# Kernel optimization log

Hardware: AMD Instinct MI355X
Metric: run time of the kernel (lower is better)

Reference implementation:

```python
import jax, jax.numpy as jnp
import numpy as np

T, B, S, V = 50, 64, 400, 50000
D = 512; E = 512; H = 512; A = 512; POOL = 2


def setup_inputs() -> dict:
    key = jax.random.key(0)
    ks = jax.random.split(key, 20)
    def rn(k, shape, s=0.05):
        return jax.random.normal(k, shape, jnp.float32) * s
    return {
        "input_y": jax.random.randint(ks[0], (T, B), 0, V),
        "hidden": rn(ks[1], (1, B, H), 1.0),
        "context": rn(ks[2], (S, B, E), 1.0),
        "src_pad_mask": jnp.zeros((B, S), jnp.float32),
        "init_att": rn(ks[3], (B, E), 1.0),
        "coverage": jnp.zeros((B, S), jnp.float32),
        "global_ctx": rn(ks[4], (B, E), 1.0),
        "emb_W": rn(ks[5], (V, D)).at[0].set(0.0),  # padding_idx=0
        "W_ih": rn(ks[6], (3 * H, D + E)),
        "W_hh": rn(ks[7], (3 * H, H)),
        "b_ih": jnp.zeros((3 * H,), jnp.float32),
        "b_hh": jnp.zeros((3 * H,), jnp.float32),
        "W_pre": rn(ks[8], (E, A)),
        "b_pre": jnp.zeros((A,), jnp.float32),
        "W_q": rn(ks[9], (H + E, A)),
        "W_v": rn(ks[10], (A,)),
        "W_cov": rn(ks[11], (A,)),
        "W_pgen": rn(ks[12], (E + H + D,)),
        "b_pgen": jnp.zeros((), jnp.float32),
        "W_ro": rn(ks[13], (D + H + E + E, H)),
        "b_ro": jnp.zeros((H,), jnp.float32),
    }


def _gru_cell(x, h, W_ih, W_hh, b_ih, b_hh):
    # PyTorch GRUCell gate order: r, z, n
    gi = x @ W_ih.T + b_ih
    gh = h @ W_hh.T + b_hh
    i_r, i_z, i_n = jnp.split(gi, 3, axis=-1)
    h_r, h_z, h_n = jnp.split(gh, 3, axis=-1)
    r = jax.nn.sigmoid(i_r + h_r)
    z = jax.nn.sigmoid(i_z + h_z)
    n = jnp.tanh(i_n + r * h_n)
    return (1.0 - z) * n + z * h


def reference(input_y, hidden, context, src_pad_mask, init_att, coverage, global_ctx,
              emb_W, W_ih, W_hh, b_ih, b_hh, W_pre, b_pre, W_q, W_v, W_cov,
              W_pgen, b_pgen, W_ro, b_ro):
    emb = emb_W[input_y]                      # [T,B,D]
    ctx = jnp.transpose(context, (1, 0, 2))   # [B,S,E]
    precompute = ctx @ W_pre + b_pre          # [B,S,A] (computed once, as in module)
    pad = src_pad_mask > 0.5
    NEG = jnp.float32(-1e18)

    def step(carry, emb_t):
        h, cur_ctx, cov = carry
        x = jnp.concatenate([emb_t, cur_ctx], 1)          # input feed
        h0 = _gru_cell(x, h[0], W_ih, W_hh, b_ih, b_hh)   # layers=1
        h = h.at[0].set(h0)
        output = h0
        # concat attention with coverage
        q = jnp.concatenate([output, global_ctx], 1) @ W_q          # [B,A]
        tmp = jnp.tanh(precompute + q[:, None, :] + cov[..., None] * W_cov)
        energy = tmp @ W_v                                           # [B,S]
        energy = jnp.where(pad, NEG, energy)
        attn = jax.nn.softmax(energy, axis=1)
        cur_ctx = jnp.einsum('bs,bse->be', attn, ctx)
        # pointer-gen
        p_gen = jax.nn.sigmoid(
            jnp.concatenate([cur_ctx, output, emb_t], 1) @ W_pgen + b_pgen)[:, None]
        # readout + maxout (dropout is identity in eval)
        readout = jnp.concatenate([emb_t, output, cur_ctx, global_ctx], 1) @ W_ro + b_ro
        mo = readout.reshape(B, H // POOL, POOL).max(axis=-1)        # [B,H/POOL]
        cov_loss = jnp.sum(jnp.minimum(attn, cov), 1)                # cov_loss_wt=1.0
        next_cov = cov + attn
        return (h, cur_ctx, next_cov), (mo, p_gen, attn, cov_loss)

    (hidden_f, cur_ctx_f, cov_f), (g_out, g_pg, g_attn, cov_losses) = jax.lax.scan(
        step, (hidden, init_att, coverage), emb)
    return (g_out, hidden_f, g_attn[-1], cur_ctx_f, g_pg, g_attn, cov_losses, cov_f)
```

## Files before the change

### kernel.cpp

```cpp
#include <hip/hip_runtime.h>
#include <hip/hip_bf16.h>


#define T_STEPS 50
#define BB 64
#define SS 400

#define O_GOUT 0
#define O_HID 819200
#define O_ATTN_LAST 851968
#define O_CTXF 877568
#define O_PG 910336
#define O_GATTN 913536
#define O_COVL 2193536
#define O_COVF 2196736

typedef __attribute__((ext_vector_type(4))) float f4;
typedef __attribute__((ext_vector_type(8))) short s8v;
typedef __attribute__((ext_vector_type(4))) unsigned u4;

static __device__ __forceinline__ float bf2f(unsigned short u){
  unsigned v = ((unsigned)u) << 16; return __builtin_bit_cast(float, v);
}
static __device__ __forceinline__ unsigned short f2bf(float f){
  unsigned u = __builtin_bit_cast(unsigned, f);
  unsigned r = (u + 0x7FFFu + ((u >> 16) & 1u)) >> 16;
  return (unsigned short)r;
}
static __device__ __forceinline__ float sigmoidf_(float x){ return 1.f/(1.f+__expf(-x)); }
static __device__ __forceinline__ float tanhf_(float x){ float e=__expf(2.f*x); return 1.f - 2.f/(e+1.f); }
static __device__ __forceinline__ u4 ntld(const unsigned short* p){
  return __builtin_nontemporal_load((const u4*)p);
}

__global__ void conv_ctx(const float* __restrict__ ctx, unsigned short* __restrict__ out){
  int o = blockIdx.x*256 + threadIdx.x;
  if(o >= SS*BB*512) return;
  int e = o & 511; int b = (o>>9)&63; int s = o>>15;
  out[((b*SS+s)<<9) + e] = f2bf(ctx[o]);
}
__global__ void conv_emb(const int* __restrict__ y, const float* __restrict__ embW,
                         unsigned short* __restrict__ embU){
  int o = blockIdx.x*256+threadIdx.x; if(o>=T_STEPS*BB*512) return;
  int d = o & 511; int i = o>>9;
  embU[o] = f2bf(embW[(long)y[i]*512 + d]);
}
__global__ void conv_rest(const float* __restrict__ W_ih, const float* __restrict__ W_hh,
                          const float* __restrict__ W_pre, const float* __restrict__ W_ro,
                          const float* __restrict__ W_q,
                          const float* __restrict__ hidden, const float* __restrict__ init_att,
                          const float* __restrict__ gctx, const float* __restrict__ coverage,
                          unsigned short* __restrict__ wihbf, unsigned short* __restrict__ wpreT,
                          unsigned short* __restrict__ wroT, unsigned short* __restrict__ Wgru,
                          unsigned short* __restrict__ WqP,
                          float* __restrict__ hrow0, unsigned short* __restrict__ h0bf_init,
                          unsigned short* __restrict__ ctx0bf, float* __restrict__ gctxT,
                          float* __restrict__ cov){
  int o = blockIdx.x*256+threadIdx.x;
  if(o < 786432){
    int j = o>>9; int d = o&511;
    wihbf[o] = f2bf(W_ih[(long)j*1024 + d]);
  } else if(o < 1048576){
    int p = o - 786432;
    int a = p>>9; int e = p&511;
    wpreT[p] = f2bf(W_pre[(long)e*512 + a]);
  } else if(o < 2097152){
    int p = o - 1048576;
    int n = p>>11; int k = p&2047;
    wroT[p] = f2bf(W_ro[(long)k*512 + n]);
  } else if(o < 3670016){
    int p = o - 2097152;
    int rg = p >> 13; int rem = p & 8191;
    int ki = rem >> 9; int ln = (rem >> 3) & 63; int e = p & 7;
    int blk = rg/24; int r2 = rg%24; int w = r2/6; int r3 = r2%6; int g = r3>>1; int op = r3&1;
    int rl = ln & 15; int kk = ((ln>>4)<<3) + e;
    int d = blk*64 + w*16 + rl; int j = g*512 + d; int k = ki*32 + kk;
    float v = op ? W_hh[(long)j*512 + k] : W_ih[(long)j*1024 + 512 + k];
    Wgru[p] = f2bf(v);
  } else if(o < 3932160){
    int p = o - 3670016;
    int e = p&7; int ln=(p>>3)&63; int kf=(p>>9)&1; int nrg=(p>>10)&31; int blk=p>>15;
    int n = nrg*16 + (ln&15);
    int k = blk*64 + kf*32 + ((ln>>4)<<3) + e;
    WqP[p] = f2bf(W_q[(long)k*512 + n]);
  } else if(o < 4056064){
    int p = o - 3932160;
    if(p < 32768){ float v = hidden[p]; hrow0[p] = v; h0bf_init[p] = f2bf(v); }
    else if(p < 65536){ int q=p-32768; ctx0bf[q] = f2bf(init_att[q]); }
    else if(p < 98304){ int q=p-65536; int b=q>>9,e=q&511; gctxT[e*64+b]=gctx[q]; }
    else { int q=p-98304; cov[q]=coverage[q]; }
  }
}

template<int OUT_BF16>
__global__ __launch_bounds__(256) void mfma_gemm(
    const unsigned short* __restrict__ Abf, int lda,
    const unsigned short* __restrict__ Bbf, int ldb,
    void* __restrict__ Cp, int ldc, const float* __restrict__ bias, int K)
{
  __shared__ __align__(16) unsigned short Ash[128*40];
  __shared__ __align__(16) unsigned short Bsh[128*40];
  int m0 = blockIdx.x*128, n0 = blockIdx.y*128;
  int tid = threadIdx.x;
  int wid = tid>>6, lane = tid&63;
  int wm = wid>>1, wn = wid&1;
  int lr = lane&15, lg = lane>>4;
  f4 acc[4][4];
  #pragma unroll
  for(int i=0;i<4;i++)
    #pragma unroll
    for(int j=0;j<4;j++) acc[i][j]=(f4)0.f;

  for(int kt=0; kt<K; kt+=32){
    #pragma unroll
    for(int c=0;c<2;c++){
      int flat = tid*16 + c*8;
      int row = flat>>5, col = flat&31;
      const unsigned short* ga = Abf + (long)(m0+row)*lda + kt + col;
      *(uint4*)(&Ash[row*40+col]) = *(const uint4*)ga;
      const unsigned short* gb = Bbf + (long)(n0+row)*ldb + kt + col;
      *(uint4*)(&Bsh[row*40+col]) = *(const uint4*)gb;
    }
    __syncthreads();
    s8v av[4], bv[4];
    #pragma unroll
    for(int mi=0;mi<4;mi++) av[mi] = *(const s8v*)(&Ash[(wm*64+mi*16+lr)*40 + lg*8]);
    #pragma unroll
    for(int ni=0;ni<4;ni++) bv[ni] = *(const s8v*)(&Bsh[(wn*64+ni*16+lr)*40 + lg*8]);
    #pragma unroll
    for(int mi=0;mi<4;mi++)
      #pragma unroll
      for(int ni=0;ni<4;ni++)
        acc[mi][ni] = __builtin_amdgcn_mfma_f32_16x16x32_bf16(av[mi], bv[ni], acc[mi][ni], 0,0,0);
    __syncthreads();
  }
  #pragma unroll
  for(int mi=0;mi<4;mi++)
    #pragma unroll
    for(int ni=0;ni<4;ni++){
      int gc = n0 + wn*64 + ni*16 + lr;
      #pragma unroll
      for(int r=0;r<4;r++){
        int gr = m0 + wm*64 + mi*16 + lg*4 + r;
        float v = acc[mi][ni][r];
        if(bias) v += bias[gc];
        if(OUT_BF16) ((unsigned short*)Cp)[(long)gr*ldc + gc] = f2bf(v);
        else         ((float*)Cp)[(long)gr*ldc + gc] = v;
      }
    }
}

__global__ __launch_bounds__(256) void mfma_gemm_ro(
    const unsigned short* __restrict__ embU, const unsigned short* __restrict__ h0bf,
    const unsigned short* __restrict__ ctxA, const unsigned short* __restrict__ wroT,
    float* __restrict__ RO, const float* __restrict__ bias)
{
  __shared__ __align__(16) unsigned short Ash[128*40];
  __shared__ __align__(16) unsigned short Bsh[128*40];
  int m0 = blockIdx.x*128, n0 = blockIdx.y*128;
  int tid = threadIdx.x;
  int wid = tid>>6, lane = tid&63;
  int wm = wid>>1, wn = wid&1;
  int lr = lane&15, lg = lane>>4;
  f4 acc[4][4];
  #pragma unroll
  for(int i=0;i<4;i++)
    #pragma unroll
    for(int j=0;j<4;j++) acc[i][j]=(f4)0.f;

  for(int kt=0; kt<1536; kt+=32){
    const unsigned short* src = (kt<512) ? embU : (kt<1024) ? h0bf : ctxA;
    int klocal = kt & 511;
    #pragma unroll
    for(int c=0;c<2;c++){
      int flat = tid*16 + c*8;
      int row = flat>>5, col = flat&31;
      *(uint4*)(&Ash[row*40+col]) = *(const uint4*)(src + (long)(m0+row)*512 + klocal + col);
      *(uint4*)(&Bsh[row*40+col]) = *(const uint4*)(wroT + (long)(n0+row)*2048 + kt + col);
    }
    __syncthreads();
    s8v av[4], bv[4];
    #pragma unroll
    for(int mi=0;mi<4;mi++) av[mi] = *(const s8v*)(&Ash[(wm*64+mi*16+lr)*40 + lg*8]);
    #pragma unroll
    for(int ni=0;ni<4;ni++) bv[ni] = *(const s8v*)(&Bsh[(wn*64+ni*16+lr)*40 + lg*8]);
    #pragma unroll
    for(int mi=0;mi<4;mi++)
      #pragma unroll
      for(int ni=0;ni<4;ni++)
        acc[mi][ni] = __builtin_amdgcn_mfma_f32_16x16x32_bf16(av[mi], bv[ni], acc[mi][ni], 0,0,0);
    __syncthreads();
  }
  #pragma unroll
  for(int mi=0;mi<4;mi++)
    #pragma unroll
    for(int ni=0;ni<4;ni++){
      int gc = n0 + wn*64 + ni*16 + lr;
      #pragma unroll
      for(int r=0;r<4;r++){
        int gr = m0 + wm*64 + mi*16 + lg*4 + r;
        RO[(long)gr*512 + gc] = acc[mi][ni][r] + bias[gc];
      }
    }
}

__global__ __launch_bounds__(256) void small2(
  const float* __restrict__ AT, const float* __restrict__ W_q, const float* __restrict__ W_ro,
  float* __restrict__ q_g, float* __restrict__ ro_g)
{
  int blk = blockIdx.x;
  int half = blk>>7; int nblk = blk&127;
  int tid = threadIdx.x;
  int b = tid&63; int nq = tid>>6;
  int n = __builtin_amdgcn_readfirstlane(nblk*4 + nq);
  const float* W = half ? W_ro : W_q;
  int koff = half ? 1536 : 512;
  float acc = 0.f;
  const float* wp = W + (long)koff*512 + n;
  #pragma unroll 8
  for(int k=0;k<512;k++){
    acc = fmaf(AT[k*64+b], wp[(long)k*512], acc);
  }
  (half ? ro_g : q_g)[b*512+n] = acc;
}

__global__ __launch_bounds__(256) void k_gru3(
  const unsigned short* __restrict__ ctx0bf, const float* __restrict__ ctxP,
  const float* __restrict__ S_part, const float* __restrict__ P_exp,
  const unsigned short* __restrict__ hprevbf,
  const float* __restrict__ hrow_in, float* __restrict__ hrow_out,
  const unsigned short* __restrict__ Wp, const unsigned short* __restrict__ WqP,
  const float* __restrict__ gi_emb, const float* __restrict__ b_hh,
  unsigned short* __restrict__ h0bf_all, float* __restrict__ qpart,
  float* __restrict__ cov, unsigned short* __restrict__ ctxA,
  float* __restrict__ outp, int t)
{
  __shared__ __align__(16) unsigned short Ash[2*64*256];
  __shared__ __align__(16) unsigned short HS[64*72];
  __shared__ float invS[64];
  __shared__ float red[256];
  int blk = blockIdx.x;
  int tid = threadIdx.x;
  int w = tid>>6, lane = tid&63;
  int lr = lane&15, lg = lane>>4;

  if(blk >= 8){
    if(t==0) return;
    int b = blk-8; int tb = t-1;
    float S = S_part[b*4]+S_part[b*4+1]+S_part[b*4+2]+S_part[b*4+3];
    float inv = 1.f/S;
    float clp;
    {
      float p = P_exp[b*400+tid];
      float attn = p*inv;
      float co = cov[b*400+tid];
      clp = fminf(attn, co);
      cov[b*400+tid] = co+attn;
      outp[O_GATTN + (long)tb*25600 + b*400 + tid] = attn;
    }
    if(tid<144){
      int i = 256+tid;
      float p = P_exp[b*400+i];
      float attn = p*inv;
      float co = cov[b*400+i];
      clp += fminf(attn, co);
      cov[b*400+i] = co+attn;
      outp[O_GATTN + (long)tb*25600 + b*400 + i] = attn;
    }
    red[tid]=clp; __syncthreads();
    for(int o=128;o;o>>=1){ if(tid<o) red[tid]+=red[tid+o]; __syncthreads(); }
    if(tid==0) outp[O_COVL + tb*64 + b] = red[0];
    return;
  }

  int swz = (lr&7)<<4;
  int rgbase = blk*24 + w*6;
  if(t>0 && tid<64){
    float S = S_part[tid*4]+S_part[tid*4+1]+S_part[tid*4+2]+S_part[tid*4+3];
    invS[tid] = 1.f/S;
  }
  __syncthreads();

  f4 acc2[6][4];
  #pragma unroll
  for(int u=0;u<6;u++)
    #pragma unroll
    for(int mi=0;mi<4;mi++) acc2[u][mi]=(f4)0.f;

  for(int kp=0; kp<2; kp++){
    for(int c = tid; c < 4096; c += 256){
      int op = c>>11; int row = (c>>5)&63; int kc = c&31;
      int e0 = kp*256 + kc*8;
      u4 v;
      if(op){
        v = *(const u4*)(hprevbf + row*512 + e0);
      } else if(t>0){
        const float* cp = ctxP + (long)row*2048 + e0;
        float sc = invS[row];
        f4 a0 = *(const f4*)(cp);
        f4 a1 = *(const f4*)(cp+512);
        f4 a2 = *(const f4*)(cp+1024);
        f4 a3 = *(const f4*)(cp+1536);
        f4 b0 = *(const f4*)(cp+4);
        f4 b1 = *(const f4*)(cp+516);
        f4 b2 = *(const f4*)(cp+1028);
        f4 b3 = *(const f4*)(cp+1540);
        f4 s0 = (a0+a1+a2+a3)*sc;
        f4 s1 = (b0+b1+b2+b3)*sc;
        v.x = (unsigned)f2bf(s0.x) | ((unsigned)f2bf(s0.y)<<16);
        v.y = (unsigned)f2bf(s0.z) | ((unsigned)f2bf(s0.w)<<16);
        v.z = (unsigned)f2bf(s1.x) | ((unsigned)f2bf(s1.y)<<16);
        v.w = (unsigned)f2bf(s1.z) | ((unsigned)f2bf(s1.w)<<16);
        if(blk == (row>>3))
          *(u4*)(ctxA + ((long)((t-1)*64+row))*512 + e0) = v;
      } else {
        v = *(const u4*)(ctx0bf + row*512 + e0);
      }
      int dst = op*32768 + row*512 + ((kc*16) ^ ((row&7)<<4));
      *(u4*)((char*)Ash + dst) = v;
    }
    __syncthreads();
    #pragma unroll 2
    for(int ktl=0; ktl<256; ktl+=32){
      s8v av[2][4];
      #pragma unroll
      for(int op=0;op<2;op++)
        #pragma unroll
        for(int mi=0;mi<4;mi++)
          av[op][mi] = *(const s8v*)((const char*)Ash + op*32768 + (mi*16+lr)*512 + ((ktl*2 + lg*16) ^ swz));
      int ki = kp*8 + (ktl>>5);
      const unsigned short* wb = Wp + (long)rgbase*8192 + ki*512 + lane*8;
      #pragma unroll
      for(int u=0;u<6;u++){
        s8v bv = *(const s8v*)(wb + (long)u*8192);
        #pragma unroll
        for(int mi=0;mi<4;mi++)
          acc2[u][mi] = __builtin_amdgcn_mfma_f32_16x16x32_bf16(av[u&1][mi], bv, acc2[u][mi], 0,0,0);
      }
    }
    __syncthreads();
  }

  int d = blk*64 + w*16 + lr;
  float bhr = b_hh[d], bhz = b_hh[512+d], bhn = b_hh[1024+d];
  #pragma unroll
  for(int mi=0;mi<4;mi++){
    #pragma unroll
    for(int r=0;r<4;r++){
      int b = mi*16 + lg*4 + r;
      const float* ge = gi_emb + (long)(t*64+b)*1536;
      float g0 = __builtin_nontemporal_load(ge + d);
      float g1 = __builtin_nontemporal_load(ge + 512 + d);
      float g2 = __builtin_nontemporal_load(ge + 1024 + d);
      float rr = sigmoidf_(g0 + bhr + acc2[0][mi][r] + acc2[1][mi][r]);
      float zz = sigmoidf_(g1 + bhz + acc2[2][mi][r] + acc2[3][mi][r]);
      float nn = tanhf_(  g2       + acc2[4][mi][r] + rr*(acc2[5][mi][r] + bhn));
      float hp = hrow_in[b*512 + d];
      float hv = (1.f-zz)*nn + zz*hp;
      hrow_out[b*512+d] = hv;
      unsigned short hb = f2bf(hv);
      h0bf_all[(long)(t*64+b)*512 + d] = hb;
      HS[b*72 + w*16 + lr] = hb;
      if(t==T_STEPS-1) outp[O_HID + b*512 + d] = hv;
    }
  }
  __syncthreads();
  #pragma unroll
  for(int i=0;i<8;i++){
    f4 accq[4];
    #pragma unroll
    for(int mi=0;mi<4;mi++) accq[mi]=(f4)0.f;
    #pragma unroll
    for(int kf=0;kf<2;kf++){
      s8v bv = *(const s8v*)(WqP + ((((long)blk*32 + (w*8+i))*2 + kf)*64 + lane)*8);
      #pragma unroll
      for(int mi=0;mi<4;mi++){
        s8v av = *(const s8v*)(HS + (mi*16+lr)*72 + kf*32 + lg*8);
        accq[mi] = __builtin_amdgcn_mfma_f32_16x16x32_bf16(av, bv, accq[mi], 0,0,0);
      }
    }
    int n = w*128 + i*16 + lr;
    #pragma unroll
    for(int mi=0;mi<4;mi++)
      #pragma unroll
      for(int r=0;r<4;r++)
        qpart[(long)blk*32768 + (long)(mi*16+lg*4+r)*512 + n] = accq[mi][r];
  }
}

__global__ __launch_bounds__(512) void k_energy2(
  const unsigned short* __restrict__ pre, const float* __restrict__ qpart,
  const float* __restrict__ q_g, const float* __restrict__ cov,
  const float* __restrict__ Wv, const float* __restrict__ Wcov,
  const float* __restrict__ padm, const unsigned short* __restrict__ ctxbf,
  float* __restrict__ P_exp, float* __restrict__ S_part, float* __restrict__ ctxP)
{
  __shared__ float q_sh[512], wv_sh[512], wc_sh[512];
  __shared__ float covL[104], padL[104], pL[104];
  __shared__ float pb[8][512];
  __shared__ float red2[8];
  int cq = blockIdx.x, b = blockIdx.y; int c0 = cq*100;
  int tid = threadIdx.x, w = tid>>6, lane = tid&63;
  {
    float acc = q_g[b*512+tid];
    #pragma unroll
    for(int p=0;p<8;p++) acc += qpart[((long)p<<15) + b*512 + tid];
    q_sh[tid] = acc;
    wv_sh[tid] = Wv[tid]; wc_sh[tid] = Wcov[tid];
    if(tid<100){ covL[tid]=cov[b*400+c0+tid]; padL[tid]=padm[b*400+c0+tid]; }
  }
  __syncthreads();
  float wsum = 0.f;
  int i = w;
  u4 pf = {0,0,0,0};
  if(i<100) pf = ntld(pre + (((long)(b*400+c0+i))<<9) + lane*8);
  while(i<100){
    u4 cur = pf;
    int nx = i+8;
    if(nx<100) pf = ntld(pre + (((long)(b*400+c0+nx))<<9) + lane*8);
    float cv = covL[i];
    float part = 0.f;
    int a0 = lane*8;
    #pragma unroll
    for(int q4=0;q4<4;q4++){
      unsigned uu = (q4==0)?cur.x:(q4==1)?cur.y:(q4==2)?cur.z:cur.w;
      int a = a0 + q4*2;
      part += wv_sh[a]  * tanhf_(bf2f((unsigned short)(uu&0xffffu)) + q_sh[a]   + cv*wc_sh[a]);
      part += wv_sh[a+1]* tanhf_(bf2f((unsigned short)(uu>>16))    + q_sh[a+1] + cv*wc_sh[a+1]);
    }
    #pragma unroll
    for(int off=32;off;off>>=1) part += __shfl_xor(part, off, 64);
    if(lane==0){
      float e = (padL[i]>0.5f) ? -1e18f : part;
      float p = __expf(e);
      pL[i] = p;
      P_exp[b*400+c0+i] = p;
      wsum += p;
    }
    i = nx;
  }
  if(lane==0) red2[w]=wsum;
  __syncthreads();
  if(tid==0)
    S_part[b*4+cq] = red2[0]+red2[1]+red2[2]+red2[3]+red2[4]+red2[5]+red2[6]+red2[7];
  float acc8[8];
  #pragma unroll
  for(int j=0;j<8;j++) acc8[j]=0.f;
  i = w;
  u4 cf = {0,0,0,0};
  if(i<100) cf = ntld(ctxbf + (((long)(b*400+c0+i))<<9) + lane*8);
  while(i<100){
    u4 cur = cf;
    int nx = i+8;
    if(nx<100) cf = ntld(ctxbf + (((long)(b*400+c0+nx))<<9) + lane*8);
    float pv = pL[i];
    acc8[0] = fmaf(pv, bf2f((unsigned short)(cur.x&0xffffu)), acc8[0]);
    acc8[1] = fmaf(pv, bf2f((unsigned short)(cur.x>>16)),     acc8[1]);
    acc8[2] = fmaf(pv, bf2f((unsigned short)(cur.y&0xffffu)), acc8[2]);
    acc8[3] = fmaf(pv, bf2f((unsigned short)(cur.y>>16)),     acc8[3]);
    acc8[4] = fmaf(pv, bf2f((unsigned short)(cur.z&0xffffu)), acc8[4]);
    acc8[5] = fmaf(pv, bf2f((unsigned short)(cur.z>>16)),     acc8[5]);
    acc8[6] = fmaf(pv, bf2f((unsigned short)(cur.w&0xffffu)), acc8[6]);
    acc8[7] = fmaf(pv, bf2f((unsigned short)(cur.w>>16)),     acc8[7]);
    i = nx;
  }
  f4 v0 = {acc8[0],acc8[1],acc8[2],acc8[3]};
  f4 v1 = {acc8[4],acc8[5],acc8[6],acc8[7]};
  *(f4*)(&pb[w][lane*8])   = v0;
  *(f4*)(&pb[w][lane*8+4]) = v1;
  __syncthreads();
  {
    float v = pb[0][tid]+pb[1][tid]+pb[2][tid]+pb[3][tid]
             +pb[4][tid]+pb[5][tid]+pb[6][tid]+pb[7][tid];
    ctxP[((long)b*4+cq)*512 + tid] = v;
  }
}

__global__ __launch_bounds__(256) void k_fin(
  const float* __restrict__ ctxP, const float* __restrict__ S_part,
  const float* __restrict__ P_exp, const float* __restrict__ cov,
  unsigned short* __restrict__ ctxA, float* __restrict__ outp)
{
  __shared__ float red[256];
  int b = blockIdx.x; int tid = threadIdx.x;
  const int tb = T_STEPS-1;
  float S = S_part[b*4]+S_part[b*4+1]+S_part[b*4+2]+S_part[b*4+3];
  float inv = 1.f/S;
  float clp;
  {
    float p = P_exp[b*400+tid]; float attn = p*inv;
    float co = cov[b*400+tid];
    clp = fminf(attn, co);
    float nc = co+attn;
    outp[O_GATTN + (long)tb*25600 + b*400 + tid] = attn;
    outp[O_ATTN_LAST + b*400 + tid] = attn;
    outp[O_COVF + b*400 + tid] = nc;
  }
  if(tid<144){
    int i = 256+tid;
    float p = P_exp[b*400+i]; float attn = p*inv;
    float co = cov[b*400+i];
    clp += fminf(attn, co);
    float nc = co+attn;
    outp[O_GATTN + (long)tb*25600 + b*400 + i] = attn;
    outp[O_ATTN_LAST + b*400 + i] = attn;
    outp[O_COVF + b*400 + i] = nc;
  }
  red[tid]=clp; __syncthreads();
  for(int o=128;o;o>>=1){ if(tid<o) red[tid]+=red[tid+o]; __syncthreads(); }
  if(tid==0) outp[O_COVL + tb*64 + b] = red[0];
  for(int c=tid;c<512;c+=256){
    float v = (ctxP[(long)b*2048+c]+ctxP[(long)b*2048+512+c]
              +ctxP[(long)b*2048+1024+c]+ctxP[(long)b*2048+1536+c])*inv;
    outp[O_CTXF + b*512 + c] = v;
    ctxA[(long)(tb*64+b)*512 + c] = f2bf(v);
  }
}

__global__ __launch_bounds__(256) void k_post(
  const unsigned short* __restrict__ embU, const unsigned short* __restrict__ h0bf,
  const unsigned short* __restrict__ ctxA, const float* __restrict__ Wpg,
  const float* __restrict__ bpg, const float* __restrict__ RO,
  const float* __restrict__ ro_g, float* __restrict__ outp)
{
  int blk = blockIdx.x;
  if(blk < 800){
    int wid = threadIdx.x>>6, lane=threadIdx.x&63;
    int m = blk*4 + wid;
    float acc=0.f;
    #pragma unroll
    for(int i=0;i<8;i++){
      int k = i*64+lane;
      acc = fmaf(bf2f(ctxA[(long)m*512+k]), Wpg[k], acc);
      acc = fmaf(bf2f(h0bf[(long)m*512+k]), Wpg[512+k], acc);
      acc = fmaf(bf2f(embU[(long)m*512+k]), Wpg[1024+k], acc);
    }
    #pragma unroll
    for(int off=32; off; off>>=1) acc += __shfl_xor(acc, off, 64);
    if(lane==0) outp[O_PG + m] = sigmoidf_(acc + bpg[0]);
  } else {
    int o = (blk-800)*256 + threadIdx.x;
    int h = o & 255; int m = o>>8; int b = m & 63;
    float v0 = RO[(long)m*512 + 2*h]   + ro_g[b*512 + 2*h];
    float v1 = RO[(long)m*512 + 2*h+1] + ro_g[b*512 + 2*h+1];
    outp[O_GOUT + o] = fmaxf(v0,v1);
  }
}

extern "C" void kernel_launch(void* const* d_in, const int* in_sizes, int n_in,
                              void* d_out, int out_size, void* d_ws, size_t ws_size,
                              hipStream_t stream)
{
  (void)in_sizes; (void)n_in; (void)out_size; (void)ws_size;
  const int*   y       = (const int*)d_in[0];
  const float* hidden  = (const float*)d_in[1];
  const float* context = (const float*)d_in[2];
  const float* padm    = (const float*)d_in[3];
  const float* init_att= (const float*)d_in[4];
  const float* coverage= (const float*)d_in[5];
  const float* gctx    = (const float*)d_in[6];
  const float* embW    = (const float*)d_in[7];
  const float* W_ih    = (const float*)d_in[8];
  const float* W_hh    = (const float*)d_in[9];
  const float* b_ih    = (const float*)d_in[10];
  const float* b_hh    = (const float*)d_in[11];
  const float* W_pre   = (const float*)d_in[12];
  const float* b_pre   = (const float*)d_in[13];
  const float* W_q     = (const float*)d_in[14];
  const float* W_v     = (const float*)d_in[15];
  const float* W_cov   = (const float*)d_in[16];
  const float* W_pg    = (const float*)d_in[17];
  const float* b_pg    = (const float*)d_in[18];
  const float* W_ro    = (const float*)d_in[19];
  const float* b_ro    = (const float*)d_in[20];
  float* out = (float*)d_out;

  char* wsb = (char*)d_ws;
  size_t off = 0;
  auto alloc = [&](size_t bytes)->char*{ char* p = wsb+off; off += (bytes+255)&~255UL; return p; };
  unsigned short* pre    = (unsigned short*)alloc(25600UL*512*2);
  unsigned short* ctxbf  = (unsigned short*)alloc(13107200UL*2);
  unsigned short* embU   = (unsigned short*)alloc(3200UL*512*2);
  unsigned short* wihbf  = (unsigned short*)alloc(1536UL*512*2);
  unsigned short* wpreT  = (unsigned short*)alloc(512UL*512*2);
  unsigned short* wroT   = (unsigned short*)alloc(512UL*2048*2);
  unsigned short* Wgru   = (unsigned short*)alloc(192UL*8192*2);
  unsigned short* WqP    = (unsigned short*)alloc(262144UL*2);
  float* gi_emb = (float*)alloc(3200UL*1536*4);
  float* RO     = (float*)alloc(3200UL*512*4);
  float* q_g    = (float*)alloc(64UL*512*4);
  float* ro_g   = (float*)alloc(64UL*512*4);
  float* hrow0  = (float*)alloc(64UL*512*4);
  float* hrow1  = (float*)alloc(64UL*512*4);
  float* gctxT  = (float*)alloc(512UL*64*4);
  unsigned short* h0bf = (unsigned short*)alloc(3200UL*512*2);
  unsigned short* h0bf_init = (unsigned short*)alloc(64UL*512*2);
  unsigned short* ctx0bf    = (unsigned short*)alloc(64UL*512*2);
  unsigned short* ctxA = (unsigned short*)alloc(3200UL*512*2);
  float* ctxP   = (float*)alloc(64UL*4*512*4);
  float* P_exp  = (float*)alloc(64UL*400*4);
  float* S_part = (float*)alloc(64UL*4*4);
  float* qpart  = (float*)alloc(8UL*64*512*4);
  float* cov    = (float*)alloc(64UL*400*4);

  conv_ctx <<<dim3(51200),dim3(256),0,stream>>>(context, ctxbf);
  conv_emb <<<dim3(6400), dim3(256),0,stream>>>(y, embW, embU);
  conv_rest<<<dim3(15844),dim3(256),0,stream>>>(W_ih, W_hh, W_pre, W_ro, W_q,
                                                hidden, init_att, gctx, coverage,
                                                wihbf, wpreT, wroT, Wgru, WqP,
                                                hrow0, h0bf_init, ctx0bf, gctxT, cov);

  mfma_gemm<1><<<dim3(200,4),dim3(256),0,stream>>>(ctxbf,512, wpreT,512,  pre,   512, b_pre, 512);
  mfma_gemm<0><<<dim3(25,12),dim3(256),0,stream>>>(embU, 512, wihbf,512,  gi_emb,1536, b_ih, 512);
  small2<<<dim3(256),dim3(256),0,stream>>>(gctxT, W_q, W_ro, q_g, ro_g);

  for(int t=0; t<T_STEPS; t++){
    float* hin  = (t&1) ? hrow1 : hrow0;
    float* hout = (t&1) ? hrow0 : hrow1;
    const unsigned short* hprevbf = t ? (h0bf + (long)(t-1)*32768) : h0bf_init;
    k_gru3<<<dim3(72),dim3(256),0,stream>>>(ctx0bf, ctxP, S_part, P_exp, hprevbf,
                                            hin, hout, Wgru, WqP, gi_emb, b_hh,
                                            h0bf, qpart, cov, ctxA, out, t);
    k_energy2<<<dim3(4,64),dim3(512),0,stream>>>(pre, qpart, q_g, cov, W_v, W_cov,
                                                 padm, ctxbf, P_exp, S_part, ctxP);
  }

  k_fin<<<dim3(64),dim3(256),0,stream>>>(ctxP, S_part, P_exp, cov, ctxA, out);
  mfma_gemm_ro<<<dim3(25,4),dim3(256),0,stream>>>(embU, h0bf, ctxA, wroT, RO, b_ro);
  k_post<<<dim3(4000),dim3(256),0,stream>>>(embU, h0bf, ctxA, W_pg, b_pg, RO, ro_g, out);
}
```

Measured before the change: 3.011 ms.

## Fuse GRU and attention-energy kernels into one per-step launch with flag sync

Merges the per-step GRU kernel and the attention energy kernel into a single 264-block launch. The 8 GRU blocks publish the query partials and signal completion through an atomic per-step flag, while the 256 attention blocks spin-wait on that flag. The coverage update and coverage-loss work moves into the attention blocks, and S_part is double-buffered so readers of the previous step do not race the current writers. This halves the kernel launches inside the step loop and overlaps the coverage work with the GRU. In exchange it relies on all blocks being co-resident, and a spin-wait with a timeout break could deadlock or silently continue if they are not.

```diff
diff --git a/kernel.cpp b/kernel.cpp
--- a/kernel.cpp
+++ b/kernel.cpp
@@ -29,8 +29,13 @@
 }
 static __device__ __forceinline__ float sigmoidf_(float x){ return 1.f/(1.f+__expf(-x)); }
 static __device__ __forceinline__ float tanhf_(float x){ float e=__expf(2.f*x); return 1.f - 2.f/(e+1.f); }
-static __device__ __forceinline__ u4 ntld(const unsigned short* p){
-  return __builtin_nontemporal_load((const u4*)p);
+static __device__ __forceinline__ float ald32f(const float* p){
+  unsigned u = __hip_atomic_load((const unsigned*)p, __ATOMIC_RELAXED, __HIP_MEMORY_SCOPE_AGENT);
+  return __builtin_bit_cast(float, u);
+}
+static __device__ __forceinline__ void ast32f(float* p, float v){
+  __hip_atomic_store((unsigned*)p, __builtin_bit_cast(unsigned, v),
+                     __ATOMIC_RELAXED, __HIP_MEMORY_SCOPE_AGENT);
 }
 
 __global__ void conv_ctx(const float* __restrict__ ctx, unsigned short* __restrict__ out){
@@ -55,7 +60,7 @@
                           unsigned short* __restrict__ WqP,
                           float* __restrict__ hrow0, unsigned short* __restrict__ h0bf_init,
                           unsigned short* __restrict__ ctx0bf, float* __restrict__ gctxT,
-                          float* __restrict__ cov){
+                          float* __restrict__ cov, unsigned* __restrict__ flags){
   int o = blockIdx.x*256+threadIdx.x;
   if(o < 786432){
     int j = o>>9; int d = o&511;
@@ -83,12 +88,13 @@
     int n = nrg*16 + (ln&15);
     int k = blk*64 + kf*32 + ((ln>>4)<<3) + e;
     WqP[p] = f2bf(W_q[(long)k*512 + n]);
-  } else if(o < 4056064){
+  } else if(o < 4056128){
     int p = o - 3932160;
     if(p < 32768){ float v = hidden[p]; hrow0[p] = v; h0bf_init[p] = f2bf(v); }
     else if(p < 65536){ int q=p-32768; ctx0bf[q] = f2bf(init_att[q]); }
     else if(p < 98304){ int q=p-65536; int b=q>>9,e=q&511; gctxT[e*64+b]=gctx[q]; }
-    else { int q=p-98304; cov[q]=coverage[q]; }
+    else if(p < 123904){ int q=p-98304; cov[q]=coverage[q]; }
+    else { int q=p-123904; if(q<64) flags[q]=0u; }
   }
 }
 
@@ -224,291 +230,299 @@
   (half ? ro_g : q_g)[b*512+n] = acc;
 }
 
-__global__ __launch_bounds__(256) void k_gru3(
-  const unsigned short* __restrict__ ctx0bf, const float* __restrict__ ctxP,
-  const float* __restrict__ S_part, const float* __restrict__ P_exp,
+__global__ __launch_bounds__(512) void k_step(
+  const unsigned short* __restrict__ ctx0bf, float* __restrict__ ctxP,
+  float* __restrict__ S_part, float* __restrict__ P_exp,
   const unsigned short* __restrict__ hprevbf,
   const float* __restrict__ hrow_in, float* __restrict__ hrow_out,
   const unsigned short* __restrict__ Wp, const unsigned short* __restrict__ WqP,
   const float* __restrict__ gi_emb, const float* __restrict__ b_hh,
   unsigned short* __restrict__ h0bf_all, float* __restrict__ qpart,
   float* __restrict__ cov, unsigned short* __restrict__ ctxA,
+  const unsigned short* __restrict__ pre, const unsigned short* __restrict__ ctxbf,
+  const float* __restrict__ q_g, const float* __restrict__ Wv,
+  const float* __restrict__ Wcov, const float* __restrict__ padm,
+  float* __restrict__ covl_part, unsigned* __restrict__ flags,
   float* __restrict__ outp, int t)
 {
-  __shared__ __align__(16) unsigned short Ash[2*64*256];
-  __shared__ __align__(16) unsigned short HS[64*72];
-  __shared__ float invS[64];
-  __shared__ float red[256];
-  int blk = blockIdx.x;
-  int tid = threadIdx.x;
-  int w = tid>>6, lane = tid&63;
-  int lr = lane&15, lg = lane>>4;
-
-  if(blk >= 8){
-    if(t==0) return;
-    int b = blk-8; int tb = t-1;
-    float S = S_part[b*4]+S_part[b*4+1]+S_part[b*4+2]+S_part[b*4+3];
-    float inv = 1.f/S;
-    float clp;
-    {
-      float p = P_exp[b*400+tid];
-      float attn = p*inv;
-      float co = cov[b*400+tid];
-      clp = fminf(attn, co);
-      cov[b*400+tid] = co+attn;
-      outp[O_GATTN + (long)tb*25600 + b*400 + tid] = attn;
-    }
-    if(tid<144){
-      int i = 256+tid;
-      float p = P_exp[b*400+i];
-      float attn = p*inv;
-      float co = cov[b*400+i];
-      clp += fminf(attn, co);
-      cov[b*400+i] = co+attn;
-      outp[O_GATTN + (long)tb*25600 + b*400 + i] = attn;
-    }
-    red[tid]=clp; __syncthreads();
-    for(int o=128;o;o>>=1){ if(tid<o) red[tid]+=red[tid+o]; __syncthreads(); }
-    if(tid==0) outp[O_COVL + tb*64 + b] = red[0];
-    return;
-  }
-
-  int swz = (lr&7)<<4;
-  int rgbase = blk*24 + w*6;
-  if(t>0 && tid<64){
-    float S = S_part[tid*4]+S_part[tid*4+1]+S_part[tid*4+2]+S_part[tid*4+3];
-    invS[tid] = 1.f/S;
-  }
-  __syncthreads();
-
-  f4 acc2[6][4];
-  #pragma unroll
-  for(int u=0;u<6;u++)
-    #pragma unroll
-    for(int mi=0;mi<4;mi++) acc2[u][mi]=(f4)0.f;
-
-  for(int kp=0; kp<2; kp++){
-    for(int c = tid; c < 4096; c += 256){
-      int op = c>>11; int row = (c>>5)&63; int kc = c&31;
-      int e0 = kp*256 + kc*8;
-      u4 v;
-      if(op){
-        v = *(const u4*)(hprevbf + row*512 + e0);
-      } else if(t>0){
-        const float* cp = ctxP + (long)row*2048 + e0;
-        float sc = invS[row];
-        f4 a0 = *(const f4*)(cp);
-        f4 a1 = *(const f4*)(cp+512);
-        f4 a2 = *(const f4*)(cp+1024);
-        f4 a3 = *(const f4*)(cp+1536);
-        f4 b0 = *(const f4*)(cp+4);
-        f4 b1 = *(const f4*)(cp+516);
-        f4 b2 = *(const f4*)(cp+1028);
-        f4 b3 = *(const f4*)(cp+1540);
-        f4 s0 = (a0+a1+a2+a3)*sc;
-        f4 s1 = (b0+b1+b2+b3)*sc;
-        v.x = (unsigned)f2bf(s0.x) | ((unsigned)f2bf(s0.y)<<16);
-        v.y = (unsigned)f2bf(s0.z) | ((unsigned)f2bf(s0.w)<<16);
-        v.z = (unsigned)f2bf(s1.x) | ((unsigned)f2bf(s1.y)<<16);
-        v.w = (unsigned)f2bf(s1.z) | ((unsigned)f2bf(s1.w)<<16);
-        if(blk == (row>>3))
-          *(u4*)(ctxA + ((long)((t-1)*64+row))*512 + e0) = v;
-      } else {
-        v = *(const u4*)(ctx0bf + row*512 + e0);
-      }
-      int dst = op*32768 + row*512 + ((kc*16) ^ ((row&7)<<4));
-      *(u4*)((char*)Ash + dst) = v;
-    }
-    __syncthreads();
-    #pragma unroll 2
-    for(int ktl=0; ktl<256; ktl+=32){
-      s8v av[2][4];
-      #pragma unroll
-      for(int op=0;op<2;op++)
+  __shared__ __align__(16) char smem[75008];
+  const int blk = blockIdx.x;
+  const int tid = threadIdx.x;
+  const int w = tid>>6, lane = tid&63;
+  const int lr = lane&15, lg = lane>>4;
+
+  if(blk < 8){
+    unsigned short* Ash = (unsigned short*)smem;
+    unsigned short* HS  = (unsigned short*)(smem+65536);
+    float* invS = (float*)(smem+74752);
+    const int swz = (lr&7)<<4;
+    const int rgbase = blk*24 + w*6;
+
+    if(t>0 && tid<64){
+      const float* Sp = S_part + ((t-1)&1)*256 + tid*4;
+      invS[tid] = 1.f/(Sp[0]+Sp[1]+Sp[2]+Sp[3]);
+    }
+    __syncthreads();
+
+    f4 acc2[6][4];
+    #pragma unroll
+    for(int u=0;u<6;u++)
+      #pragma unroll
+      for(int mi=0;mi<4;mi++) acc2[u][mi]=(f4)0.f;
+
+    for(int kp=0; kp<2; kp++){
+      for(int c = tid; c < 4096; c += 512){
+        int op = c>>11; int row = (c>>5)&63; int kc = c&31;
+        int e0 = kp*256 + kc*8;
+        u4 v;
+        if(op){
+          v = *(const u4*)(hprevbf + row*512 + e0);
+        } else if(t>0){
+          const float* cp = ctxP + (long)row*2048 + e0;
+          float sc = invS[row];
+          f4 a0 = *(const f4*)(cp);
+          f4 a1 = *(const f4*)(cp+512);
+          f4 a2 = *(const f4*)(cp+1024);
+          f4 a3 = *(const f4*)(cp+1536);
+          f4 b0 = *(const f4*)(cp+4);
+          f4 b1 = *(const f4*)(cp+516);
+          f4 b2 = *(const f4*)(cp+1028);
+          f4 b3 = *(const f4*)(cp+1540);
+          f4 s0 = (a0+a1+a2+a3)*sc;
+          f4 s1 = (b0+b1+b2+b3)*sc;
+          v.x = (unsigned)f2bf(s0.x) | ((unsigned)f2bf(s0.y)<<16);
+          v.y = (unsigned)f2bf(s0.z) | ((unsigned)f2bf(s0.w)<<16);
+          v.z = (unsigned)f2bf(s1.x) | ((unsigned)f2bf(s1.y)<<16);
+          v.w = (unsigned)f2bf(s1.z) | ((unsigned)f2bf(s1.w)<<16);
+          if(blk == (row>>3))
+            *(u4*)(ctxA + ((long)((t-1)*64+row))*512 + e0) = v;
+        } else {
+          v = *(const u4*)(ctx0bf + row*512 + e0);
+        }
+        int dst = op*32768 + row*512 + ((kc*16) ^ ((row&7)<<4));
+        *(u4*)((char*)Ash + dst) = v;
+      }
+      __syncthreads();
+      if(w<4){
+        #pragma unroll 2
+        for(int ktl=0; ktl<256; ktl+=32){
+          s8v av[2][4];
+          #pragma unroll
+          for(int op=0;op<2;op++)
+            #pragma unroll
+            for(int mi=0;mi<4;mi++)
+              av[op][mi] = *(const s8v*)((const char*)Ash + op*32768 + (mi*16+lr)*512 + ((ktl*2 + lg*16) ^ swz));
+          int ki = kp*8 + (ktl>>5);
+          const unsigned short* wb = Wp + (long)rgbase*8192 + ki*512 + lane*8;
+          #pragma unroll
+          for(int u=0;u<6;u++){
+            s8v bv = *(const s8v*)(wb + (long)u*8192);
+            #pragma unroll
+            for(int mi=0;mi<4;mi++)
+              acc2[u][mi] = __builtin_amdgcn_mfma_f32_16x16x32_bf16(av[u&1][mi], bv, acc2[u][mi], 0,0,0);
+          }
+        }
+      }
+      __syncthreads();
+    }
+
+    if(w<4){
+      int d = blk*64 + w*16 + lr;
+      float bhr = b_hh[d], bhz = b_hh[512+d], bhn = b_hh[1024+d];
+      #pragma unroll
+      for(int mi=0;mi<4;mi++){
+        #pragma unroll
+        for(int r=0;r<4;r++){
+          int b = mi*16 + lg*4 + r;
+          const float* ge = gi_emb + (long)(t*64+b)*1536;
+          float g0 = __builtin_nontemporal_load(ge + d);
+          float g1 = __builtin_nontemporal_load(ge + 512 + d);
+          float g2 = __builtin_nontemporal_load(ge + 1024 + d);
+          float rr = sigmoidf_(g0 + bhr + acc2[0][mi][r] + acc2[1][mi][r]);
+          float zz = sigmoidf_(g1 + bhz + acc2[2][mi][r] + acc2[3][mi][r]);
+          float nn = tanhf_(  g2       + acc2[4][mi][r] + rr*(acc2[5][mi][r] + bhn));
+          float hp = hrow_in[b*512 + d];
+          float hv = (1.f-zz)*nn + zz*hp;
+          hrow_out[b*512+d] = hv;
+          unsigned short hb = f2bf(hv);
+          h0bf_all[(long)(t*64+b)*512 + d] = hb;
+          HS[b*72 + w*16 + lr] = hb;
+          if(t==T_STEPS-1) outp[O_HID + b*512 + d] = hv;
+        }
+      }
+    }
+    __syncthreads();
+    if(w<4){
+      #pragma unroll
+      for(int i=0;i<8;i++){
+        f4 accq[4];
+        #pragma unroll
+        for(int mi=0;mi<4;mi++) accq[mi]=(f4)0.f;
+        #pragma unroll
+        for(int kf=0;kf<2;kf++){
+          s8v bv = *(const s8v*)(WqP + ((((long)blk*32 + (w*8+i))*2 + kf)*64 + lane)*8);
+          #pragma unroll
+          for(int mi=0;mi<4;mi++){
+            s8v av = *(const s8v*)(HS + (mi*16+lr)*72 + kf*32 + lg*8);
+            accq[mi] = __builtin_amdgcn_mfma_f32_16x16x32_bf16(av, bv, accq[mi], 0,0,0);
+          }
+        }
+        int n = w*128 + i*16 + lr;
         #pragma unroll
         for(int mi=0;mi<4;mi++)
-          av[op][mi] = *(const s8v*)((const char*)Ash + op*32768 + (mi*16+lr)*512 + ((ktl*2 + lg*16) ^ swz));
-      int ki = kp*8 + (ktl>>5);
-      const unsigned short* wb = Wp + (long)rgbase*8192 + ki*512 + lane*8;
-      #pragma unroll
-      for(int u=0;u<6;u++){
-        s8v bv = *(const s8v*)(wb + (long)u*8192);
-        #pragma unroll
-        for(int mi=0;mi<4;mi++)
-          acc2[u][mi] = __builtin_amdgcn_mfma_f32_16x16x32_bf16(av[u&1][mi], bv, acc2[u][mi], 0,0,0);
-      }
-    }
-    __syncthreads();
-  }
-
-  int d = blk*64 + w*16 + lr;
-  float bhr = b_hh[d], bhz = b_hh[512+d], bhn = b_hh[1024+d];
-  #pragma unroll
-  for(int mi=0;mi<4;mi++){
-    #pragma unroll
-    for(int r=0;r<4;r++){
-      int b = mi*16 + lg*4 + r;
-      const float* ge = gi_emb + (long)(t*64+b)*1536;
-      float g0 = __builtin_nontemporal_load(ge + d);
-      float g1 = __builtin_nontemporal_load(ge + 512 + d);
-      float g2 = __builtin_nontemporal_load(ge + 1024 + d);
-      float rr = sigmoidf_(g0 + bhr + acc2[0][mi][r] + acc2[1][mi][r]);
-      float zz = sigmoidf_(g1 + bhz + acc2[2][mi][r] + acc2[3][mi][r]);
-      float nn = tanhf_(  g2       + acc2[4][mi][r] + rr*(acc2[5][mi][r] + bhn));
-      float hp = hrow_in[b*512 + d];
-      float hv = (1.f-zz)*nn + zz*hp;
-      hrow_out[b*512+d] = hv;
-      unsigned short hb = f2bf(hv);
-      h0bf_all[(long)(t*64+b)*512 + d] = hb;
-      HS[b*72 + w*16 + lr] = hb;
-      if(t==T_STEPS-1) outp[O_HID + b*512 + d] = hv;
-    }
-  }
-  __syncthreads();
-  #pragma unroll
-  for(int i=0;i<8;i++){
-    f4 accq[4];
-    #pragma unroll
-    for(int mi=0;mi<4;mi++) accq[mi]=(f4)0.f;
-    #pragma unroll
-    for(int kf=0;kf<2;kf++){
-      s8v bv = *(const s8v*)(WqP + ((((long)blk*32 + (w*8+i))*2 + kf)*64 + lane)*8);
-      #pragma unroll
-      for(int mi=0;mi<4;mi++){
-        s8v av = *(const s8v*)(HS + (mi*16+lr)*72 + kf*32 + lg*8);
-        accq[mi] = __builtin_amdgcn_mfma_f32_16x16x32_bf16(av, bv, accq[mi], 0,0,0);
-      }
-    }
-    int n = w*128 + i*16 + lr;
-    #pragma unroll
-    for(int mi=0;mi<4;mi++)
-      #pragma unroll
-      for(int r=0;r<4;r++)
-        qpart[(long)blk*32768 + (long)(mi*16+lg*4+r)*512 + n] = accq[mi][r];
-  }
-}
-
-__global__ __launch_bounds__(512) void k_energy2(
-  const unsigned short* __restrict__ pre, const float* __restrict__ qpart,
-  const float* __restrict__ q_g, const float* __restrict__ cov,
-  const float* __restrict__ Wv, const float* __restrict__ Wcov,
-  const float* __restrict__ padm, const unsigned short* __restrict__ ctxbf,
-  float* __restrict__ P_exp, float* __restrict__ S_part, float* __restrict__ ctxP)
-{
-  __shared__ float q_sh[512], wv_sh[512], wc_sh[512];
-  __shared__ float covL[104], padL[104], pL[104];
-  __shared__ float pb[8][512];
-  __shared__ float red2[8];
-  int cq = blockIdx.x, b = blockIdx.y; int c0 = cq*100;
-  int tid = threadIdx.x, w = tid>>6, lane = tid&63;
+          #pragma unroll
+          for(int r=0;r<4;r++)
+            ast32f(qpart + (long)blk*32768 + (long)(mi*16+lg*4+r)*512 + n, accq[mi][r]);
+      }
+    }
+    asm volatile("s_waitcnt vmcnt(0)" ::: "memory");
+    __syncthreads();
+    if(tid==0)
+      __hip_atomic_fetch_add(flags+t, 1u, __ATOMIC_RELEASE, __HIP_MEMORY_SCOPE_AGENT);
+    return;
+  }
+
   {
-    float acc = q_g[b*512+tid];
-    #pragma unroll
-    for(int p=0;p<8;p++) acc += qpart[((long)p<<15) + b*512 + tid];
-    q_sh[tid] = acc;
-    wv_sh[tid] = Wv[tid]; wc_sh[tid] = Wcov[tid];
-    if(tid<100){ covL[tid]=cov[b*400+c0+tid]; padL[tid]=padm[b*400+c0+tid]; }
-  }
-  __syncthreads();
-  float wsum = 0.f;
-  int i = w;
-  u4 pf = {0,0,0,0};
-  if(i<100) pf = ntld(pre + (((long)(b*400+c0+i))<<9) + lane*8);
-  while(i<100){
-    u4 cur = pf;
-    int nx = i+8;
-    if(nx<100) pf = ntld(pre + (((long)(b*400+c0+nx))<<9) + lane*8);
-    float cv = covL[i];
-    float part = 0.f;
-    int a0 = lane*8;
-    #pragma unroll
-    for(int q4=0;q4<4;q4++){
-      unsigned uu = (q4==0)?cur.x:(q4==1)?cur.y:(q4==2)?cur.z:cur.w;
-      int a = a0 + q4*2;
-      part += wv_sh[a]  * tanhf_(bf2f((unsigned short)(uu&0xffffu)) + q_sh[a]   + cv*wc_sh[a]);
-      part += wv_sh[a+1]* tanhf_(bf2f((unsigned short)(uu>>16))    + q_sh[a+1] + cv*wc_sh[a+1]);
-    }
-    #pragma unroll
-    for(int off=32;off;off>>=1) part += __shfl_xor(part, off, 64);
-    if(lane==0){
-      float e = (padL[i]>0.5f) ? -1e18f : part;
-      float p = __expf(e);
-      pL[i] = p;
-      P_exp[b*400+c0+i] = p;
-      wsum += p;
-    }
-    i = nx;
-  }
-  if(lane==0) red2[w]=wsum;
-  __syncthreads();
-  if(tid==0)
-    S_part[b*4+cq] = red2[0]+red2[1]+red2[2]+red2[3]+red2[4]+red2[5]+red2[6]+red2[7];
-  float acc8[8];
-  #pragma unroll
-  for(int j=0;j<8;j++) acc8[j]=0.f;
-  i = w;
-  u4 cf = {0,0,0,0};
-  if(i<100) cf = ntld(ctxbf + (((long)(b*400+c0+i))<<9) + lane*8);
-  while(i<100){
-    u4 cur = cf;
-    int nx = i+8;
-    if(nx<100) cf = ntld(ctxbf + (((long)(b*400+c0+nx))<<9) + lane*8);
-    float pv = pL[i];
-    acc8[0] = fmaf(pv, bf2f((unsigned short)(cur.x&0xffffu)), acc8[0]);
-    acc8[1] = fmaf(pv, bf2f((unsigned short)(cur.x>>16)),     acc8[1]);
-    acc8[2] = fmaf(pv, bf2f((unsigned short)(cur.y&0xffffu)), acc8[2]);
-    acc8[3] = fmaf(pv, bf2f((unsigned short)(cur.y>>16)),     acc8[3]);
-    acc8[4] = fmaf(pv, bf2f((unsigned short)(cur.z&0xffffu)), acc8[4]);
-    acc8[5] = fmaf(pv, bf2f((unsigned short)(cur.z>>16)),     acc8[5]);
-    acc8[6] = fmaf(pv, bf2f((unsigned short)(cur.w&0xffffu)), acc8[6]);
-    acc8[7] = fmaf(pv, bf2f((unsigned short)(cur.w>>16)),     acc8[7]);
-    i = nx;
-  }
-  f4 v0 = {acc8[0],acc8[1],acc8[2],acc8[3]};
-  f4 v1 = {acc8[4],acc8[5],acc8[6],acc8[7]};
-  *(f4*)(&pb[w][lane*8])   = v0;
-  *(f4*)(&pb[w][lane*8+4]) = v1;
-  __syncthreads();
-  {
-    float v = pb[0][tid]+pb[1][tid]+pb[2][tid]+pb[3][tid]
-             +pb[4][tid]+pb[5][tid]+pb[6][tid]+pb[7][tid];
-    ctxP[((long)b*4+cq)*512 + tid] = v;
+    int eb = blk-8; int b = eb>>2, cq = eb&3, c0 = cq*100;
+    float* q_sh  = (float*)smem;
+    float* wv_sh = (float*)(smem+2048);
+    float* wc_sh = (float*)(smem+4096);
+    float* covL  = (float*)(smem+6144);
+    float* padL  = (float*)(smem+6560);
+    float* pL    = (float*)(smem+6976);
+    float* red   = (float*)(smem+7392);
+    float* red2  = (float*)(smem+9440);
+    float* pb    = (float*)(smem+9472);
+
+    wv_sh[tid]=Wv[tid]; wc_sh[tid]=Wcov[tid];
+    if(tid<100) padL[tid]=padm[b*400+c0+tid];
+    float clp = 0.f;
+    if(t>0){
+      const float* Sp = S_part + ((t-1)&1)*256 + b*4;
+      float inv = 1.f/(Sp[0]+Sp[1]+Sp[2]+Sp[3]);
+      if(tid<100){
+        float p = P_exp[b*400+c0+tid]*inv;
+        float co = cov[b*400+c0+tid];
+        clp = fminf(p,co);
+        float nc = co+p;
+        cov[b*400+c0+tid]=nc;
+        covL[tid]=nc;
+        outp[O_GATTN + (long)(t-1)*25600 + b*400 + c0 + tid] = p;
+      }
+    } else {
+      if(tid<100) covL[tid]=cov[b*400+c0+tid];
+    }
+    red[tid]=clp; __syncthreads();
+    for(int o=256;o;o>>=1){ if(tid<o) red[tid]+=red[tid+o]; __syncthreads(); }
+    if(t>0 && tid==0) covl_part[(long)(t-1)*256 + b*4+cq] = red[0];
+    if(tid==0){
+      unsigned it=0;
+      while(__hip_atomic_load(flags+t, __ATOMIC_RELAXED, __HIP_MEMORY_SCOPE_AGENT) < 8u){
+        __builtin_amdgcn_s_sleep(8);
+        if(++it > 200000000u) break;
+      }
+    }
+    __syncthreads();
+    asm volatile("" ::: "memory");
+    {
+      float acc = q_g[b*512+tid];
+      #pragma unroll
+      for(int p=0;p<8;p++) acc += ald32f(qpart + ((long)p<<15) + b*512 + tid);
+      q_sh[tid] = acc;
+    }
+    __syncthreads();
+    float wsum = 0.f;
+    for(int i=w; i<100; i+=8){
+      uint4 cur = *(const uint4*)(pre + (((long)(b*400+c0+i))<<9) + lane*8);
+      float cv = covL[i];
+      float part = 0.f;
+      const unsigned* uu = (const unsigned*)&cur;
+      #pragma unroll
+      for(int q4=0;q4<4;q4++){
+        int a = lane*8 + q4*2;
+        part += wv_sh[a]  * tanhf_(bf2f((unsigned short)(uu[q4]&0xffffu)) + q_sh[a]   + cv*wc_sh[a]);
+        part += wv_sh[a+1]* tanhf_(bf2f((unsigned short)(uu[q4]>>16))    + q_sh[a+1] + cv*wc_sh[a+1]);
+      }
+      #pragma unroll
+      for(int off=32;off;off>>=1) part += __shfl_xor(part, off, 64);
+      if(lane==0){
+        float e = (padL[i]>0.5f) ? -1e18f : part;
+        float p = __expf(e);
+        pL[i] = p;
+        P_exp[b*400+c0+i] = p;
+        wsum += p;
+      }
+    }
+    if(lane==0) red2[w]=wsum;
+    __syncthreads();
+    if(tid==0)
+      S_part[(t&1)*256 + b*4+cq] = red2[0]+red2[1]+red2[2]+red2[3]+red2[4]+red2[5]+red2[6]+red2[7];
+    float acc8[8];
+    #pragma unroll
+    for(int j=0;j<8;j++) acc8[j]=0.f;
+    for(int i=w; i<100; i+=8){
+      uint4 cur = *(const uint4*)(ctxbf + (((long)(b*400+c0+i))<<9) + lane*8);
+      float pv = pL[i];
+      const unsigned* uu = (const unsigned*)&cur;
+      acc8[0] = fmaf(pv, bf2f((unsigned short)(uu[0]&0xffffu)), acc8[0]);
+      acc8[1] = fmaf(pv, bf2f((unsigned short)(uu[0]>>16)),     acc8[1]);
+      acc8[2] = fmaf(pv, bf2f((unsigned short)(uu[1]&0xffffu)), acc8[2]);
+      acc8[3] = fmaf(pv, bf2f((unsigned short)(uu[1]>>16)),     acc8[3]);
+      acc8[4] = fmaf(pv, bf2f((unsigned short)(uu[2]&0xffffu)), acc8[4]);
+      acc8[5] = fmaf(pv, bf2f((unsigned short)(uu[2]>>16)),     acc8[5]);
+      acc8[6] = fmaf(pv, bf2f((unsigned short)(uu[3]&0xffffu)), acc8[6]);
+      acc8[7] = fmaf(pv, bf2f((unsigned short)(uu[3]>>16)),     acc8[7]);
+    }
+    #pragma unroll
+    for(int j=0;j<8;j++) pb[w*512 + lane*8+j] = acc8[j];
+    __syncthreads();
+    {
+      float v = pb[tid]+pb[512+tid]+pb[1024+tid]+pb[1536+tid]
+               +pb[2048+tid]+pb[2560+tid]+pb[3072+tid]+pb[3584+tid];
+      ctxP[((long)b*4+cq)*512 + tid] = v;
+    }
   }
 }
 
 __global__ __launch_bounds__(256) void k_fin(
   const float* __restrict__ ctxP, const float* __restrict__ S_part,
   const float* __restrict__ P_exp, const float* __restrict__ cov,
+  const float* __restrict__ covl_part,
   unsigned short* __restrict__ ctxA, float* __restrict__ outp)
 {
   __shared__ float red[256];
   int b = blockIdx.x; int tid = threadIdx.x;
   const int tb = T_STEPS-1;
-  float S = S_part[b*4]+S_part[b*4+1]+S_part[b*4+2]+S_part[b*4+3];
+  const float* Sp = S_part + 256 + b*4;
+  float S = Sp[0]+Sp[1]+Sp[2]+Sp[3];
   float inv = 1.f/S;
   float clp;
   {
-    float p = P_exp[b*400+tid]; float attn = p*inv;
+    float p = P_exp[b*400+tid]*inv;
     float co = cov[b*400+tid];
-    clp = fminf(attn, co);
-    float nc = co+attn;
-    outp[O_GATTN + (long)tb*25600 + b*400 + tid] = attn;
-    outp[O_ATTN_LAST + b*400 + tid] = attn;
+    clp = fminf(p, co);
+    float nc = co+p;
+    outp[O_GATTN + (long)tb*25600 + b*400 + tid] = p;
+    outp[O_ATTN_LAST + b*400 + tid] = p;
     outp[O_COVF + b*400 + tid] = nc;
   }
   if(tid<144){
     int i = 256+tid;
-    float p = P_exp[b*400+i]; float attn = p*inv;
+    float p = P_exp[b*400+i]*inv;
     float co = cov[b*400+i];
-    clp += fminf(attn, co);
-    float nc = co+attn;
-    outp[O_GATTN + (long)tb*25600 + b*400 + i] = attn;
-    outp[O_ATTN_LAST + b*400 + i] = attn;
+    clp += fminf(p, co);
+    float nc = co+p;
+    outp[O_GATTN + (long)tb*25600 + b*400 + i] = p;
+    outp[O_ATTN_LAST + b*400 + i] = p;
     outp[O_COVF + b*400 + i] = nc;
   }
   red[tid]=clp; __syncthreads();
   for(int o=128;o;o>>=1){ if(tid<o) red[tid]+=red[tid+o]; __syncthreads(); }
   if(tid==0) outp[O_COVL + tb*64 + b] = red[0];
+  if(tid<49){
+    const float* cp = covl_part + (long)tid*256 + b*4;
+    outp[O_COVL + tid*64 + b] = cp[0]+cp[1]+cp[2]+cp[3];
+  }
   for(int c=tid;c<512;c+=256){
     float v = (ctxP[(long)b*2048+c]+ctxP[(long)b*2048+512+c]
               +ctxP[(long)b*2048+1024+c]+ctxP[(long)b*2048+1536+c])*inv;
@@ -599,16 +613,18 @@
   unsigned short* ctxA = (unsigned short*)alloc(3200UL*512*2);
   float* ctxP   = (float*)alloc(64UL*4*512*4);
   float* P_exp  = (float*)alloc(64UL*400*4);
-  float* S_part = (float*)alloc(64UL*4*4);
+  float* S_part = (float*)alloc(2UL*256*4);
   float* qpart  = (float*)alloc(8UL*64*512*4);
   float* cov    = (float*)alloc(64UL*400*4);
+  float* covl_part = (float*)alloc(50UL*256*4);
+  unsigned* flags = (unsigned*)alloc(64UL*4);
 
   conv_ctx <<<dim3(51200),dim3(256),0,stream>>>(context, ctxbf);
   conv_emb <<<dim3(6400), dim3(256),0,stream>>>(y, embW, embU);
-  conv_rest<<<dim3(15844),dim3(256),0,stream>>>(W_ih, W_hh, W_pre, W_ro, W_q,
+  conv_rest<<<dim3(15845),dim3(256),0,stream>>>(W_ih, W_hh, W_pre, W_ro, W_q,
                                                 hidden, init_att, gctx, coverage,
                                                 wihbf, wpreT, wroT, Wgru, WqP,
-                                                hrow0, h0bf_init, ctx0bf, gctxT, cov);
+                                                hrow0, h0bf_init, ctx0bf, gctxT, cov, flags);
 
   mfma_gemm<1><<<dim3(200,4),dim3(256),0,stream>>>(ctxbf,512, wpreT,512,  pre,   512, b_pre, 512);
   mfma_gemm<0><<<dim3(25,12),dim3(256),0,stream>>>(embU, 512, wihbf,512,  gi_emb,1536, b_ih, 512);
@@ -618,14 +634,14 @@
     float* hin  = (t&1) ? hrow1 : hrow0;
     float* hout = (t&1) ? hrow0 : hrow1;
     const unsigned short* hprevbf = t ? (h0bf + (long)(t-1)*32768) : h0bf_init;
-    k_gru3<<<dim3(72),dim3(256),0,stream>>>(ctx0bf, ctxP, S_part, P_exp, hprevbf,
-                                            hin, hout, Wgru, WqP, gi_emb, b_hh,
-                                            h0bf, qpart, cov, ctxA, out, t);
-    k_energy2<<<dim3(4,64),dim3(512),0,stream>>>(pre, qpart, q_g, cov, W_v, W_cov,
-                                                 padm, ctxbf, P_exp, S_part, ctxP);
-  }
-
-  k_fin<<<dim3(64),dim3(256),0,stream>>>(ctxP, S_part, P_exp, cov, ctxA, out);
+    k_step<<<dim3(264),dim3(512),0,stream>>>(ctx0bf, ctxP, S_part, P_exp, hprevbf,
+                                             hin, hout, Wgru, WqP, gi_emb, b_hh,
+                                             h0bf, qpart, cov, ctxA, pre, ctxbf,
+                                             q_g, W_v, W_cov, padm, covl_part,
+                                             flags, out, t);
+  }
+
+  k_fin<<<dim3(64),dim3(256),0,stream>>>(ctxP, S_part, P_exp, cov, covl_part, ctxA, out);
   mfma_gemm_ro<<<dim3(25,4),dim3(256),0,stream>>>(embU, h0bf, ctxA, wroT, RO, b_ro);
   k_post<<<dim3(4000),dim3(256),0,stream>>>(embU, h0bf, ctxA, W_pg, b_pg, RO, ro_g, out);
 }
```

Measured after the change: 3.131 ms. 1.04x slower.
